# Kernel tuning notes

Hardware: AMD Instinct MI355X
Metric: run time of the kernel (lower is better)

## Reference

```python
import jax, jax.numpy as jnp
import numpy as np
import math

D_MODEL = 1024
N_HEAD = 16
HEAD_DIM = D_MODEL // N_HEAD
BATCH = 4
MAX_LEN = 1024


def _shift(BD):
    # BD: (b, h, L, 2L) -> (b, h, L, L), Transformer-XL relative shift
    b, h, L, _ = BD.shape
    zero_pad = jnp.zeros((b, h, L, 1), BD.dtype)
    BD = jnp.concatenate([BD, zero_pad], axis=-1)      # (b,h,L,2L+1)
    BD = BD.reshape(b, h, -1, L)[:, :, :-1]            # (b,h,2L,L)
    BD = BD.reshape(b, h, L, -1)                       # (b,h,L,2L)
    return BD[:, :, :, L:]                             # (b,h,L,L)


def setup_inputs() -> dict:
    key = jax.random.key(0)
    ks = jax.random.split(key, 10)
    s = 1.0 / math.sqrt(D_MODEL)
    return {
        "q": jax.random.normal(ks[0], (BATCH, MAX_LEN, D_MODEL), jnp.float32),
        "k": jax.random.normal(ks[1], (BATCH, MAX_LEN, D_MODEL), jnp.float32),
        "mask": jax.random.randint(ks[2], (BATCH, MAX_LEN), 0, 2, jnp.int32),
        "pos_embed": jax.random.normal(ks[3], (2 * MAX_LEN, HEAD_DIM), jnp.float32),
        "Wq": jax.random.normal(ks[4], (D_MODEL, D_MODEL), jnp.float32) * s,
        "Wkv": jax.random.normal(ks[5], (D_MODEL, 2 * D_MODEL), jnp.float32) * s,
        "Wr": jax.random.normal(ks[6], (HEAD_DIM, HEAD_DIM), jnp.float32) / math.sqrt(HEAD_DIM),
        "r_r_bias": jax.random.normal(ks[7], (N_HEAD, HEAD_DIM), jnp.float32) * 0.02,
        "r_w_bias": jax.random.normal(ks[8], (N_HEAD, HEAD_DIM), jnp.float32) * 0.02,
    }


def reference(q, k, mask, pos_embed, Wq, Wkv, Wr, r_r_bias, r_w_bias):
    B, L, D = q.shape
    H = r_r_bias.shape[0]
    hd = D // H
    scale = math.sqrt(hd)

    r = pos_embed @ Wr                                   # (2L, hd)
    qh = (q @ Wq).reshape(B, L, H, hd).transpose(0, 2, 1, 3)   # (B,H,L,hd)
    kv = k @ Wkv                                         # (B,L,2D)
    kk, vv = jnp.split(kv, 2, axis=-1)
    kh = kk.reshape(B, L, H, hd).transpose(0, 2, 1, 3)
    vh = vv.reshape(B, L, H, hd).transpose(0, 2, 1, 3)

    AC = jnp.einsum('bhqd,bhkd->bhqk', qh + r_r_bias[None, :, None, :], kh)
    BD = jnp.einsum('bhqd,ld->bhql', qh + r_w_bias[None, :, None, :], r)  # (B,H,L,2L)
    BD = _shift(BD)

    attn = (AC + BD) / scale
    attn = jnp.where(mask[:, None, None, :] == 0, -jnp.inf, attn)
    attn = jax.nn.softmax(attn, axis=-1)

    out = jnp.einsum('bhqk,bhkd->bhqd', attn, vh)        # (B,H,L,hd)
    return out.transpose(0, 2, 1, 3).reshape(B, L, D)
```

## Files before the change

### kernel.cpp

```cpp
#include <hip/hip_runtime.h>

typedef short bf16x8 __attribute__((ext_vector_type(8)));
typedef float f32x4 __attribute__((ext_vector_type(4)));
typedef unsigned short u16;
typedef unsigned short u16x4 __attribute__((ext_vector_type(4)));
typedef unsigned short u16x8 __attribute__((ext_vector_type(8)));

#define NB 4
#define LEN 1024
#define DM 1024
#define NH 16
#define HD 64

#define QSCALE 0.18033688011112043f

__device__ __forceinline__ u16 f2bf(float f) {
    union { float f; unsigned u; } v; v.f = f;
    return (u16)((v.u + 0x7fffu + ((v.u >> 16) & 1u)) >> 16);
}

__device__ __forceinline__ float exp2f_fast(float x) {
    float r; asm("v_exp_f32 %0, %1" : "=v"(r) : "v"(x)); return r;
}

__device__ __forceinline__ unsigned cvt_pk_bf16(float a, float b) {
    unsigned r; asm("v_cvt_pk_bf16_f32 %0, %1, %2" : "=v"(r) : "v"(a), "v"(b)); return r;
}

__device__ __forceinline__ f32x4 mfma16(bf16x8 a, bf16x8 b, f32x4 c) {
    return __builtin_amdgcn_mfma_f32_16x16x32_bf16(a, b, c, 0, 0, 0);
}

__device__ __forceinline__ void gload16(const void* g, void* l) {
    __builtin_amdgcn_global_load_lds(
        (const __attribute__((address_space(1))) unsigned int*)g,
        (__attribute__((address_space(3))) unsigned int*)l, 16, 0, 0);
}

__global__ void cast_all(const float* __restrict__ q, const float* __restrict__ k,
                         const int* __restrict__ msk,
                         u16* __restrict__ qbf, u16* __restrict__ kbf,
                         float* __restrict__ mb) {
    int idx = blockIdx.x * 256 + threadIdx.x;
    if (idx < 1048576) {
        float4 v = ((const float4*)q)[idx];
        u16x4 o;
        o[0] = f2bf(v.x); o[1] = f2bf(v.y); o[2] = f2bf(v.z); o[3] = f2bf(v.w);
        ((u16x4*)qbf)[idx] = o;
    } else if (idx < 2097152) {
        int i = idx - 1048576;
        float4 v = ((const float4*)k)[i];
        u16x4 o;
        o[0] = f2bf(v.x); o[1] = f2bf(v.y); o[2] = f2bf(v.z); o[3] = f2bf(v.w);
        ((u16x4*)kbf)[i] = o;
    } else {
        int i = idx - 2097152;
        if (i < NB * LEN) mb[i] = msk[i] ? 0.f : -3.0e38f;
    }
}

__global__ void transWT(const float* __restrict__ Wq, const float* __restrict__ Wkv,
                        u16* __restrict__ WqT, u16* __restrict__ WkvT) {
    __shared__ float tile[32][33];
    const bool isQ = blockIdx.x < 32;
    const float* W = isQ ? Wq : Wkv;
    u16* WT = isQ ? WqT : WkvT;
    const int N = isQ ? 1024 : 2048;
    const int n0 = (isQ ? blockIdx.x : blockIdx.x - 32) * 32;
    const int k0 = blockIdx.y * 32;
    int tx = threadIdx.x, ty = threadIdx.y;
    #pragma unroll
    for (int j = 0; j < 4; j++) {
        int r = ty + j * 8;
        tile[r][tx] = W[(size_t)(k0 + r) * N + n0 + tx];
    }
    __syncthreads();
    #pragma unroll
    for (int j = 0; j < 4; j++) {
        int r = ty + j * 8;
        WT[(size_t)(n0 + r) * 1024 + k0 + tx] = f2bf(tile[tx][r]);
    }
}

__global__ void r_proj(const float* __restrict__ pos, const float* __restrict__ Wr,
                       u16* __restrict__ rbf) {
    int idx = blockIdx.x * 256 + threadIdx.x;
    if (idx >= 2064 * 64) return;
    int row = idx >> 6, col = idx & 63;
    float s = 0.f;
    if (row < 2048) {
        #pragma unroll
        for (int kk = 0; kk < 64; kk++) s += pos[row * 64 + kk] * Wr[kk * 64 + col];
    }
    const int csw = (((col >> 3) ^ (row & 7)) << 3) | (col & 7);
    rbf[(row << 6) | csw] = f2bf(s);
}

__global__ __launch_bounds__(256) void gemm_all(
    const u16* __restrict__ qbf, const u16* __restrict__ kbf,
    const u16* __restrict__ WqT, const u16* __restrict__ WkvT,
    const float* __restrict__ rrb, const float* __restrict__ rwb,
    u16* __restrict__ A1, u16* __restrict__ A2,
    u16* __restrict__ khs, u16* __restrict__ vhsT)
{
    __shared__ u16 as[2][128][32];
    __shared__ u16 bs[2][128][32];

    const int bx = blockIdx.x;
    const bool isQ = bx < 8;
    const u16* Abf = isQ ? qbf : kbf;
    const u16* BT  = isQ ? WqT : WkvT;
    const int n0 = (isQ ? bx : bx - 8) * 128;
    const int m0 = blockIdx.y * 128;
    const int tid = threadIdx.x;
    const int w = tid >> 6, lane = tid & 63, g = lane >> 4, c = lane & 15;
    const int wm = w >> 1, wn = w & 1;
    const int srow = lane >> 2, sj = lane & 3;

    const f32x4 fzero = {0.f, 0.f, 0.f, 0.f};
    f32x4 acc[4][4];
    #pragma unroll
    for (int i = 0; i < 4; i++)
        #pragma unroll
        for (int j = 0; j < 4; j++) acc[i][j] = fzero;

    auto STAGE = [&](int buf, int ks) {
        const int k0 = ks * 32;
        #pragma unroll
        for (int i = 0; i < 2; i++) {
            const int rb = w * 32 + i * 16;
            const int rowA = rb + srow;
            gload16(Abf + (size_t)(m0 + rowA) * 1024 + k0 + ((sj ^ (rowA & 3)) << 3),
                    &as[buf][rb][0]);
            gload16(BT + (size_t)(n0 + rowA) * 1024 + k0 + ((sj ^ (rowA & 3)) << 3),
                    &bs[buf][rb][0]);
        }
    };

    STAGE(0, 0);
    __syncthreads();

    for (int ks = 0; ks < 32; ks++) {
        const int cur = ks & 1, nb = cur ^ 1;
        if (ks < 31) STAGE(nb, ks + 1);

        bf16x8 af[4], bfr[4];
        #pragma unroll
        for (int i = 0; i < 4; i++) {
            const int row = wm * 64 + i * 16 + c;
            af[i] = *(const bf16x8*)&as[cur][row][(g ^ (row & 3)) << 3];
        }
        #pragma unroll
        for (int j = 0; j < 4; j++) {
            const int row = wn * 64 + j * 16 + c;
            bfr[j] = *(const bf16x8*)&bs[cur][row][(g ^ (row & 3)) << 3];
        }
        #pragma unroll
        for (int i = 0; i < 4; i++)
            #pragma unroll
            for (int j = 0; j < 4; j++)
                acc[i][j] = mfma16(af[i], bfr[j], acc[i][j]);

        __syncthreads();
    }

    #pragma unroll
    for (int j = 0; j < 4; j++) {
        const int n = n0 + wn * 64 + j * 16 + c;
        float b1v = 0.f, b2v = 0.f;
        if (isQ) { b1v = rrb[n]; b2v = rwb[n]; }
        #pragma unroll
        for (int i = 0; i < 4; i++) {
            const int l0 = m0 + wm * 64 + i * 16 + 4 * g;
            if (!isQ && n >= DM) {
                const int d = n & 63, hh = (n - DM) >> 6;
                const int bb = l0 >> 10, l = l0 & 1023;
                u16x4 o;
                #pragma unroll
                for (int r = 0; r < 4; r++) o[r] = f2bf(acc[i][j][r]);
                *(u16x4*)(vhsT + (((size_t)(bb * NH + hh)) * HD + d) * LEN + l) = o;
            } else {
                #pragma unroll
                for (int r = 0; r < 4; r++) {
                    const int row = l0 + r;
                    const int bb = row >> 10, l = row & 1023;
                    const float v = acc[i][j][r];
                    if (isQ) {
                        size_t idx = (((size_t)(bb * NH + (n >> 6))) * LEN + l) * HD + (n & 63);
                        A1[idx] = f2bf((v + b1v) * QSCALE);
                        A2[idx] = f2bf((v + b2v) * QSCALE);
                    } else {
                        const int d = n & 63;
                        const int dsw = (((d >> 3) ^ (l & 7)) << 3) | (d & 7);
                        size_t idx = (((size_t)(bb * NH + (n >> 6))) * LEN + l) * HD + dsw;
                        khs[idx] = f2bf(v);
                    }
                }
            }
        }
    }
}

__global__ __launch_bounds__(256, 2) void attn_kernel(
    const u16* __restrict__ A1, const u16* __restrict__ A2,
    const u16* __restrict__ khs, const u16* __restrict__ vhsT,
    const u16* __restrict__ rbf, const float* __restrict__ mbias,
    float* __restrict__ outp)
{
    __shared__ u16 kbuf[2][32][64];
    __shared__ u16 rbuf[192][64];
    __shared__ u16 vbuf[2][4][64][8];
    __shared__ float biasl[1024];
    __shared__ float gl[4][2][16][52];
    __shared__ u16 pl[4][32][40];

    const int bh = blockIdx.x;
    const int b = bh >> 4, h = bh & 15;
    const int tid = threadIdx.x;
    const int w = tid >> 6, lane = tid & 63, g = lane >> 4, c = lane & 15;
    const int q0 = blockIdx.y * 128, q0w = q0 + w * 32;
    const int lrow8 = lane >> 3, lcol = lane & 7;
    const int kkey = (c + 1) & 7;

    const u16* Kbase = khs + (size_t)bh * LEN * HD;
    const u16* Vp = vhsT + (size_t)bh * HD * LEN;
    u16* plw = &pl[w][0][0];

    const u16* A1p = A1 + ((size_t)bh * LEN + q0w) * HD;
    const u16* A2p = A2 + ((size_t)bh * LEN + q0w) * HD;
    bf16x8 a1f[2][2], a2f[2][2];
    #pragma unroll
    for (int qs = 0; qs < 2; qs++)
        #pragma unroll
        for (int kf = 0; kf < 2; kf++) {
            a1f[qs][kf] = *(const bf16x8*)(A1p + (qs * 16 + c) * HD + kf * 32 + g * 8);
            a2f[qs][kf] = *(const bf16x8*)(A2p + (qs * 16 + c) * HD + kf * 32 + g * 8);
        }

    gload16(mbias + b * LEN + w * 256 + lane * 4, &biasl[w * 256]);
    gload16(Kbase + (((size_t)(w * 8 + lrow8)) << 6) + (lcol << 3), &kbuf[0][w * 8][0]);
    gload16(Vp + ((size_t)lane << 10) + w * 8, &vbuf[0][w][0][0]);
    const int js0 = LEN - q0 - 128;
    #pragma unroll
    for (int i = 0; i < 5; i++) {
        const int jg = js0 + (w + 4 * i) * 8;
        gload16(rbf + (((size_t)(jg + lrow8)) << 6) + (lcol << 3), &rbuf[jg % 192][0]);
    }
    __syncthreads();

    int psl = (js0 + 160) % 192;
    int bsl = (LEN - q0w - 31) % 192;

    const f32x4 fzero = {0.f, 0.f, 0.f, 0.f};
    f32x4 oacc[2][4];
    #pragma unroll
    for (int qs = 0; qs < 2; qs++)
        #pragma unroll
        for (int dt = 0; dt < 4; dt++) oacc[qs][dt] = fzero;
    float mrow[2] = {-3.0e38f, -3.0e38f}, lrow[2] = {0.f, 0.f};

    for (int kt = 0; kt < 32; kt++) {
        const int cur = kt & 1, nb = cur ^ 1;
        const int c0 = kt * 32;

        if (kt < 31) {
            const int c0n = c0 + 32;
            gload16(Kbase + (((size_t)(c0n + w * 8 + lrow8)) << 6) + (lcol << 3), &kbuf[nb][w * 8][0]);
            gload16(Vp + ((size_t)lane << 10) + c0n + w * 8, &vbuf[nb][w][0][0]);
            const int pg = js0 + 160 + 32 * kt + 8 * w;
            int ps = psl + 8 * w; if (ps >= 192) ps -= 192;
            gload16(rbf + (((size_t)(pg + lrow8)) << 6) + (lcol << 3), &rbuf[ps][0]);
        }

        bf16x8 Kf[2][2];
        #pragma unroll
        for (int ct = 0; ct < 2; ct++)
            #pragma unroll
            for (int kf = 0; kf < 2; kf++)
                Kf[ct][kf] = *(const bf16x8*)&kbuf[cur][16 * ct + c][((4 * kf + g) ^ (c & 7)) * 8];

        bf16x8 Rf[4][2];
        #pragma unroll
        for (int mt = 0; mt < 4; mt++) {
            int t = bsl + mt * 16 + c; if (t >= 192) t -= 192;
            #pragma unroll
            for (int kf = 0; kf < 2; kf++)
                Rf[mt][kf] = *(const bf16x8*)&rbuf[t][((4 * kf + g) ^ kkey) * 8];
        }

        f32x4 s[2][2];
        #pragma unroll
        for (int qs = 0; qs < 2; qs++)
            #pragma unroll
            for (int ct = 0; ct < 2; ct++) {
                f32x4 a = fzero;
                a = mfma16(Kf[ct][0], a1f[qs][0], a);
                a = mfma16(Kf[ct][1], a1f[qs][1], a);
                s[qs][ct] = a;
            }

        #pragma unroll
        for (int mt = 1; mt < 4; mt++) {
            f32x4 ga = fzero;
            ga = mfma16(Rf[mt][0], a2f[0][0], ga);
            ga = mfma16(Rf[mt][1], a2f[0][1], ga);
            *(f32x4*)&gl[w][0][c][(mt - 1) * 16 + 4 * g] = ga;
        }
        #pragma unroll
        for (int mt = 0; mt < 3; mt++) {
            f32x4 ga = fzero;
            ga = mfma16(Rf[mt][0], a2f[1][0], ga);
            ga = mfma16(Rf[mt][1], a2f[1][1], ga);
            *(f32x4*)&gl[w][1][c][mt * 16 + 4 * g] = ga;
        }

        const float* glq0 = &gl[w][0][c][0];
        const float* glq1 = &gl[w][1][c][0];
        f32x4 bb0 = *(const f32x4*)&biasl[c0 + 4 * g];
        f32x4 bb1 = *(const f32x4*)&biasl[c0 + 16 + 4 * g];
        #pragma unroll
        for (int r = 0; r < 4; r++) {
            const int gidx = 4 * g + r + 15 - c;
            s[0][0][r] += glq0[gidx] + bb0[r];
            s[0][1][r] += glq0[gidx + 16] + bb1[r];
            s[1][0][r] += glq1[gidx] + bb0[r];
            s[1][1][r] += glq1[gidx + 16] + bb1[r];
        }

        bf16x8 Vb[4];
        #pragma unroll
        for (int dt = 0; dt < 4; dt++)
            Vb[dt] = *(const bf16x8*)&vbuf[cur][g][16 * dt + c][0];

        #pragma unroll
        for (int qs = 0; qs < 2; qs++) {
            float t = fmaxf(fmaxf(fmaxf(s[qs][0][0], s[qs][0][1]), fmaxf(s[qs][0][2], s[qs][0][3])),
                            fmaxf(fmaxf(s[qs][1][0], s[qs][1][1]), fmaxf(s[qs][1][2], s[qs][1][3])));
            t = fmaxf(t, __shfl_xor(t, 16));
            t = fmaxf(t, __shfl_xor(t, 32));
            if (!__all(t <= mrow[qs] + 8.f)) {
                const float mnew = fmaxf(mrow[qs], t);
                const float alpha = exp2f_fast(mrow[qs] - mnew);
                mrow[qs] = mnew;
                lrow[qs] *= alpha;
                #pragma unroll
                for (int dt = 0; dt < 4; dt++)
                    #pragma unroll
                    for (int r = 0; r < 4; r++) oacc[qs][dt][r] *= alpha;
            }
            const float mref = mrow[qs];
            float p[8];
            float ps = 0.f;
            #pragma unroll
            for (int r = 0; r < 4; r++) {
                p[r] = exp2f_fast(s[qs][0][r] - mref);
                p[4 + r] = exp2f_fast(s[qs][1][r] - mref);
                ps += p[r] + p[4 + r];
            }
            lrow[qs] += ps;
            const unsigned d0 = cvt_pk_bf16(p[0], p[1]);
            const unsigned d1 = cvt_pk_bf16(p[2], p[3]);
            const unsigned d2 = cvt_pk_bf16(p[4], p[5]);
            const unsigned d3 = cvt_pk_bf16(p[6], p[7]);
            const int prow = (qs * 16 + c) * 40;
            *(uint2*)&plw[prow + 4 * g] = make_uint2(d0, d1);
            *(uint2*)&plw[prow + 16 + 4 * g] = make_uint2(d2, d3);
            bf16x8 pbr = *(const bf16x8*)&plw[prow + 8 * g];
            #pragma unroll
            for (int dt = 0; dt < 4; dt++)
                oacc[qs][dt] = mfma16(Vb[dt], pbr, oacc[qs][dt]);
        }

        psl += 32; if (psl >= 192) psl -= 192;
        bsl += 32; if (bsl >= 192) bsl -= 192;
        __syncthreads();
    }

    #pragma unroll
    for (int qs = 0; qs < 2; qs++) {
        float sum = lrow[qs];
        sum += __shfl_xor(sum, 16);
        sum += __shfl_xor(sum, 32);
        const float inv = sum > 0.f ? 1.0f / sum : 0.f;
        const int l = q0w + qs * 16 + c;
        float* op = outp + ((size_t)b * LEN + l) * DM + h * HD;
        #pragma unroll
        for (int dt = 0; dt < 4; dt++) {
            f32x4 o;
            #pragma unroll
            for (int r = 0; r < 4; r++) o[r] = oacc[qs][dt][r] * inv;
            *(f32x4*)(op + dt * 16 + 4 * g) = o;
        }
    }
}

extern "C" void kernel_launch(void* const* d_in, const int* in_sizes, int n_in,
                              void* d_out, int out_size, void* d_ws, size_t ws_size,
                              hipStream_t stream) {
    const float* q   = (const float*)d_in[0];
    const float* k   = (const float*)d_in[1];
    const int*   msk = (const int*)d_in[2];
    const float* pos = (const float*)d_in[3];
    const float* Wq  = (const float*)d_in[4];
    const float* Wkv = (const float*)d_in[5];
    const float* Wr  = (const float*)d_in[6];
    const float* rrb = (const float*)d_in[7];
    const float* rwb = (const float*)d_in[8];
    float* outp = (float*)d_out;
    char* ws = (char*)d_ws;

    u16* qbf  = (u16*)(ws + 0);
    u16* kbf  = (u16*)(ws + 8388608);
    u16* WqT  = (u16*)(ws + 16777216);
    u16* WkvT = (u16*)(ws + 18874368);
    u16* rbf  = (u16*)(ws + 23068672);
    u16* A1   = (u16*)(ws + 23332864);
    u16* A2   = (u16*)(ws + 31721472);
    u16* khs  = (u16*)(ws + 40110080);
    u16* vhsT = (u16*)(ws + 48498688);
    float* mb = (float*)(ws + 56887296);

    cast_all<<<8208, 256, 0, stream>>>(q, k, msk, qbf, kbf, mb);
    transWT<<<dim3(96, 32), dim3(32, 8), 0, stream>>>(Wq, Wkv, WqT, WkvT);
    r_proj<<<516, 256, 0, stream>>>(pos, Wr, rbf);
    gemm_all<<<dim3(24, 32), 256, 0, stream>>>(qbf, kbf, WqT, WkvT, rrb, rwb, A1, A2, khs, vhsT);
    attn_kernel<<<dim3(64, 8), 256, 0, stream>>>(A1, A2, khs, vhsT, rbf, mb, outp);
}
```

Measured before the change: 124.7 us.

## Merge prep kernels, swizzle GEMM blocks, reuse R fragments, add MFMA priority

Folds the cast, weight-transpose and r-projection kernels into one prep launch to cut launch overhead. Remaps gemm block indices so consecutive blocks are spread across XCDs. In the attention loop, reuses two of the four R fragments from the previous step by unrolling the loop by two with ping-pong register sets, and raises wave priority around the MFMA sections. This adds register pressure and a more complex loop body.

```diff
diff --git a/kernel.cpp b/kernel.cpp
--- a/kernel.cpp
+++ b/kernel.cpp
@@ -5,6 +5,7 @@
 typedef unsigned short u16;
 typedef unsigned short u16x4 __attribute__((ext_vector_type(4)));
 typedef unsigned short u16x8 __attribute__((ext_vector_type(8)));
+typedef unsigned int u32;
 
 #define NB 4
 #define LEN 1024
@@ -37,63 +38,66 @@
         (__attribute__((address_space(3))) unsigned int*)l, 16, 0, 0);
 }
 
-__global__ void cast_all(const float* __restrict__ q, const float* __restrict__ k,
-                         const int* __restrict__ msk,
-                         u16* __restrict__ qbf, u16* __restrict__ kbf,
-                         float* __restrict__ mb) {
-    int idx = blockIdx.x * 256 + threadIdx.x;
-    if (idx < 1048576) {
-        float4 v = ((const float4*)q)[idx];
-        u16x4 o;
-        o[0] = f2bf(v.x); o[1] = f2bf(v.y); o[2] = f2bf(v.z); o[3] = f2bf(v.w);
-        ((u16x4*)qbf)[idx] = o;
-    } else if (idx < 2097152) {
-        int i = idx - 1048576;
-        float4 v = ((const float4*)k)[i];
-        u16x4 o;
-        o[0] = f2bf(v.x); o[1] = f2bf(v.y); o[2] = f2bf(v.z); o[3] = f2bf(v.w);
-        ((u16x4*)kbf)[i] = o;
+__global__ void prep(const float* __restrict__ q, const float* __restrict__ k,
+                     const int* __restrict__ msk,
+                     const float* __restrict__ Wq, const float* __restrict__ Wkv,
+                     const float* __restrict__ pos, const float* __restrict__ Wr,
+                     u16* __restrict__ qbf, u16* __restrict__ kbf,
+                     u16* __restrict__ WqT, u16* __restrict__ WkvT,
+                     u16* __restrict__ rbf, float* __restrict__ mb) {
+    __shared__ float tile[32][33];
+    const int f = blockIdx.x;
+    const int tid = threadIdx.x;
+    if (f < 3072) {
+        const int x = f % 96, y = f / 96;
+        const bool isQ = x < 32;
+        const float* W = isQ ? Wq : Wkv;
+        u16* WT = isQ ? WqT : WkvT;
+        const int N = isQ ? 1024 : 2048;
+        const int n0 = (isQ ? x : x - 32) * 32;
+        const int k0 = y * 32;
+        const int tx = tid & 31, ty = tid >> 5;
+        #pragma unroll
+        for (int j = 0; j < 4; j++) {
+            int r = ty + j * 8;
+            tile[r][tx] = W[(size_t)(k0 + r) * N + n0 + tx];
+        }
+        __syncthreads();
+        #pragma unroll
+        for (int j = 0; j < 4; j++) {
+            int r = ty + j * 8;
+            WT[(size_t)(n0 + r) * 1024 + k0 + tx] = f2bf(tile[tx][r]);
+        }
+    } else if (f < 3588) {
+        int idx = (f - 3072) * 256 + tid;
+        if (idx < 2064 * 64) {
+            int row = idx >> 6, col = idx & 63;
+            float s = 0.f;
+            if (row < 2048) {
+                #pragma unroll
+                for (int kk = 0; kk < 64; kk++) s += pos[row * 64 + kk] * Wr[kk * 64 + col];
+            }
+            const int csw = (((col >> 3) ^ (row & 7)) << 3) | (col & 7);
+            rbf[(row << 6) | csw] = f2bf(s);
+        }
+    } else if (f < 3604) {
+        int i = (f - 3588) * 256 + tid;
+        if (i < NB * LEN) mb[i] = msk[i] ? 0.f : -3.0e38f;
     } else {
-        int i = idx - 2097152;
-        if (i < NB * LEN) mb[i] = msk[i] ? 0.f : -3.0e38f;
-    }
-}
-
-__global__ void transWT(const float* __restrict__ Wq, const float* __restrict__ Wkv,
-                        u16* __restrict__ WqT, u16* __restrict__ WkvT) {
-    __shared__ float tile[32][33];
-    const bool isQ = blockIdx.x < 32;
-    const float* W = isQ ? Wq : Wkv;
-    u16* WT = isQ ? WqT : WkvT;
-    const int N = isQ ? 1024 : 2048;
-    const int n0 = (isQ ? blockIdx.x : blockIdx.x - 32) * 32;
-    const int k0 = blockIdx.y * 32;
-    int tx = threadIdx.x, ty = threadIdx.y;
-    #pragma unroll
-    for (int j = 0; j < 4; j++) {
-        int r = ty + j * 8;
-        tile[r][tx] = W[(size_t)(k0 + r) * N + n0 + tx];
-    }
-    __syncthreads();
-    #pragma unroll
-    for (int j = 0; j < 4; j++) {
-        int r = ty + j * 8;
-        WT[(size_t)(n0 + r) * 1024 + k0 + tx] = f2bf(tile[tx][r]);
-    }
-}
-
-__global__ void r_proj(const float* __restrict__ pos, const float* __restrict__ Wr,
-                       u16* __restrict__ rbf) {
-    int idx = blockIdx.x * 256 + threadIdx.x;
-    if (idx >= 2064 * 64) return;
-    int row = idx >> 6, col = idx & 63;
-    float s = 0.f;
-    if (row < 2048) {
-        #pragma unroll
-        for (int kk = 0; kk < 64; kk++) s += pos[row * 64 + kk] * Wr[kk * 64 + col];
-    }
-    const int csw = (((col >> 3) ^ (row & 7)) << 3) | (col & 7);
-    rbf[(row << 6) | csw] = f2bf(s);
+        int idx = (f - 3604) * 256 + tid;
+        if (idx < 1048576) {
+            float4 v = ((const float4*)q)[idx];
+            u16x4 o;
+            o[0] = f2bf(v.x); o[1] = f2bf(v.y); o[2] = f2bf(v.z); o[3] = f2bf(v.w);
+            ((u16x4*)qbf)[idx] = o;
+        } else if (idx < 2097152) {
+            int i = idx - 1048576;
+            float4 v = ((const float4*)k)[i];
+            u16x4 o;
+            o[0] = f2bf(v.x); o[1] = f2bf(v.y); o[2] = f2bf(v.z); o[3] = f2bf(v.w);
+            ((u16x4*)kbf)[i] = o;
+        }
+    }
 }
 
 __global__ __launch_bounds__(256) void gemm_all(
@@ -106,12 +110,14 @@
     __shared__ u16 as[2][128][32];
     __shared__ u16 bs[2][128][32];
 
-    const int bx = blockIdx.x;
+    const int fb = blockIdx.x;
+    const int wsw = ((fb & 7) * 96) + (fb >> 3);
+    const int bx = wsw % 24;
     const bool isQ = bx < 8;
     const u16* Abf = isQ ? qbf : kbf;
     const u16* BT  = isQ ? WqT : WkvT;
     const int n0 = (isQ ? bx : bx - 8) * 128;
-    const int m0 = blockIdx.y * 128;
+    const int m0 = (wsw / 24) * 128;
     const int tid = threadIdx.x;
     const int w = tid >> 6, lane = tid & 63, g = lane >> 4, c = lane & 15;
     const int wm = w >> 1, wn = w & 1;
@@ -251,6 +257,15 @@
     int psl = (js0 + 160) % 192;
     int bsl = (LEN - q0w - 31) % 192;
 
+    bf16x8 RA[2][2], RB[2][2];
+    #pragma unroll
+    for (int mt = 0; mt < 2; mt++) {
+        int t = bsl + mt * 16 + c; if (t >= 192) t -= 192;
+        #pragma unroll
+        for (int kf = 0; kf < 2; kf++)
+            RA[mt][kf] = *(const bf16x8*)&rbuf[t][((4 * kf + g) ^ kkey) * 8];
+    }
+
     const f32x4 fzero = {0.f, 0.f, 0.f, 0.f};
     f32x4 oacc[2][4];
     #pragma unroll
@@ -259,7 +274,7 @@
         for (int dt = 0; dt < 4; dt++) oacc[qs][dt] = fzero;
     float mrow[2] = {-3.0e38f, -3.0e38f}, lrow[2] = {0.f, 0.f};
 
-    for (int kt = 0; kt < 32; kt++) {
+    auto STEP = [&](int kt, bf16x8 (&Rold)[2][2], bf16x8 (&Rnew)[2][2]) {
         const int cur = kt & 1, nb = cur ^ 1;
         const int c0 = kt * 32;
 
@@ -281,13 +296,18 @@
 
         bf16x8 Rf[4][2];
         #pragma unroll
-        for (int mt = 0; mt < 4; mt++) {
-            int t = bsl + mt * 16 + c; if (t >= 192) t -= 192;
-            #pragma unroll
-            for (int kf = 0; kf < 2; kf++)
-                Rf[mt][kf] = *(const bf16x8*)&rbuf[t][((4 * kf + g) ^ kkey) * 8];
-        }
-
+        for (int kf = 0; kf < 2; kf++) { Rf[0][kf] = Rold[0][kf]; Rf[1][kf] = Rold[1][kf]; }
+        #pragma unroll
+        for (int mt = 0; mt < 2; mt++) {
+            int t = bsl + 32 + mt * 16 + c; if (t >= 192) t -= 192;
+            #pragma unroll
+            for (int kf = 0; kf < 2; kf++) {
+                Rf[2 + mt][kf] = *(const bf16x8*)&rbuf[t][((4 * kf + g) ^ kkey) * 8];
+                Rnew[mt][kf] = Rf[2 + mt][kf];
+            }
+        }
+
+        __builtin_amdgcn_s_setprio(1);
         f32x4 s[2][2];
         #pragma unroll
         for (int qs = 0; qs < 2; qs++)
@@ -298,7 +318,6 @@
                 a = mfma16(Kf[ct][1], a1f[qs][1], a);
                 s[qs][ct] = a;
             }
-
         #pragma unroll
         for (int mt = 1; mt < 4; mt++) {
             f32x4 ga = fzero;
@@ -313,6 +332,7 @@
             ga = mfma16(Rf[mt][1], a2f[1][1], ga);
             *(f32x4*)&gl[w][1][c][mt * 16 + 4 * g] = ga;
         }
+        __builtin_amdgcn_s_setprio(0);
 
         const float* glq0 = &gl[w][0][c][0];
         const float* glq1 = &gl[w][1][c][0];
@@ -366,14 +386,21 @@
             *(uint2*)&plw[prow + 4 * g] = make_uint2(d0, d1);
             *(uint2*)&plw[prow + 16 + 4 * g] = make_uint2(d2, d3);
             bf16x8 pbr = *(const bf16x8*)&plw[prow + 8 * g];
+            __builtin_amdgcn_s_setprio(1);
             #pragma unroll
             for (int dt = 0; dt < 4; dt++)
                 oacc[qs][dt] = mfma16(Vb[dt], pbr, oacc[qs][dt]);
+            __builtin_amdgcn_s_setprio(0);
         }
 
         psl += 32; if (psl >= 192) psl -= 192;
         bsl += 32; if (bsl >= 192) bsl -= 192;
         __syncthreads();
+    };
+
+    for (int kt2 = 0; kt2 < 16; kt2++) {
+        STEP(2 * kt2,     RA, RB);
+        STEP(2 * kt2 + 1, RB, RA);
     }
 
     #pragma unroll
@@ -420,9 +447,7 @@
     u16* vhsT = (u16*)(ws + 48498688);
     float* mb = (float*)(ws + 56887296);
 
-    cast_all<<<8208, 256, 0, stream>>>(q, k, msk, qbf, kbf, mb);
-    transWT<<<dim3(96, 32), dim3(32, 8), 0, stream>>>(Wq, Wkv, WqT, WkvT);
-    r_proj<<<516, 256, 0, stream>>>(pos, Wr, rbf);
-    gemm_all<<<dim3(24, 32), 256, 0, stream>>>(qbf, kbf, WqT, WkvT, rrb, rwb, A1, A2, khs, vhsT);
+    prep<<<11796, 256, 0, stream>>>(q, k, msk, Wq, Wkv, pos, Wr, qbf, kbf, WqT, WkvT, rbf, mb);
+    gemm_all<<<768, 256, 0, stream>>>(qbf, kbf, WqT, WkvT, rrb, rwb, A1, A2, khs, vhsT);
     attn_kernel<<<dim3(64, 8), 256, 0, stream>>>(A1, A2, khs, vhsT, rbf, mb, outp);
 }
```

Result: faster. 118.4 us (-5.0%).
